# Kernel optimization log

Measured on AMD Instinct MI355X. Metric: run time of the kernel, lower is better.

Reference implementation:

```python
import jax, jax.numpy as jnp
import numpy as np

N = 50000
E = 1600000
IN = 128
HID = 128
OUT = 64
NL = 200000
NEG_SLOPE = 0.2


def _glorot(key, shape):
    fan_in, fan_out = shape[0], shape[-1]
    s = jnp.sqrt(6.0 / (fan_in + fan_out))
    return jax.random.uniform(key, shape, jnp.float32, -s, s)


def setup_inputs() -> dict:
    key = jax.random.key(0)
    ks = jax.random.split(key, 16)
    x = jax.random.normal(ks[0], (N, IN), jnp.float32)
    edge_index = jax.random.randint(ks[1], (2, E), 0, N, dtype=jnp.int32)
    edge_label_index = jax.random.randint(ks[2], (2, NL), 0, N, dtype=jnp.int32)
    return {
        "x": x,
        "edge_index": edge_index,
        "edge_label_index": edge_label_index,
        "W1": _glorot(ks[3], (IN, HID)),  "a1s": _glorot(ks[4], (HID,)),  "a1d": _glorot(ks[5], (HID,)),  "b1": jnp.zeros((HID,), jnp.float32),
        "W2": _glorot(ks[6], (HID, HID)), "a2s": _glorot(ks[7], (HID,)),  "a2d": _glorot(ks[8], (HID,)),  "b2": jnp.zeros((HID,), jnp.float32),
        "W3": _glorot(ks[9], (HID, HID)), "a3s": _glorot(ks[10], (HID,)), "a3d": _glorot(ks[11], (HID,)), "b3": jnp.zeros((HID,), jnp.float32),
        "W4": _glorot(ks[12], (HID, OUT)), "b4": jnp.zeros((OUT,), jnp.float32),
    }


def _add_self_loops(edge_index, n):
    loop = jnp.arange(n, dtype=edge_index.dtype)
    return jnp.concatenate([edge_index, jnp.stack([loop, loop])], axis=1)


def gat_conv(x, edge_index, W, a_s, a_d, b):
    """PyG GATConv, heads=1, add_self_loops=True: gather, LeakyReLU score,
    segment softmax over destination nodes, scatter-add aggregate."""
    n = x.shape[0]
    ei = _add_self_loops(edge_index, n)
    src, dst = ei[0], ei[1]
    h = x @ W                                    # [N, H]
    e = jax.nn.leaky_relu((h @ a_s)[src] + (h @ a_d)[dst], NEG_SLOPE)  # [E']
    m = jax.ops.segment_max(e, dst, num_segments=n)
    p = jnp.exp(e - m[dst])
    s = jax.ops.segment_sum(p, dst, num_segments=n)
    alpha = p / s[dst]                           # segment softmax
    out = jax.ops.segment_sum(h[src] * alpha[:, None], dst, num_segments=n)
    return out + b


def gcn_conv(x, edge_index, W, b):
    """PyG GCNConv: self-loops + symmetric degree normalization."""
    n = x.shape[0]
    ei = _add_self_loops(edge_index, n)
    src, dst = ei[0], ei[1]
    h = x @ W
    deg = jax.ops.segment_sum(jnp.ones(src.shape, h.dtype), dst, num_segments=n)
    dinv = jax.lax.rsqrt(deg)
    norm = dinv[src] * dinv[dst]                 # [E']
    out = jax.ops.segment_sum(h[src] * norm[:, None], dst, num_segments=n)
    return out + b


def reference(x, edge_index, edge_label_index,
              W1, a1s, a1d, b1, W2, a2s, a2d, b2,
              W3, a3s, a3d, b3, W4, b4):
    h = jax.nn.relu(gat_conv(x, edge_index, W1, a1s, a1d, b1))
    h = jax.nn.relu(gat_conv(h, edge_index, W2, a2s, a2d, b2))
    h = jax.nn.relu(gat_conv(h, edge_index, W3, a3s, a3d, b3))
    z = gcn_conv(h, edge_index, W4, b4)          # [N, OUT]
    # decode: dot product of endpoint embeddings -> link logits [NL]
    return (z[edge_label_index[0]] * z[edge_label_index[1]]).sum(axis=-1)
```

## Files before the change

kernel.cpp:

```cpp
#include <hip/hip_runtime.h>
#include <hip/hip_fp16.h>
#include <math.h>

#define NN   50000
#define NE   1600000
#define NLBL 200000
#define CAP  80
#define NEG  0.2f
#define NBK  196
#define CAPB 8800
#define CHK  4096
#define GBIN 391

typedef unsigned short u16;
typedef _Float16 half8 __attribute__((ext_vector_type(8)));
typedef float floatx4 __attribute__((ext_vector_type(4)));


__device__ void ph_bin(int blk, const int* __restrict__ ei,
                       int* __restrict__ gcnt, unsigned* __restrict__ bins) {
    __shared__ int cntL[NBK];
    __shared__ int offL[NBK];
    __shared__ int curL[NBK];
    __shared__ int curG[NBK];
    __shared__ unsigned stage[CHK];
    const int tid = threadIdx.x;
    const int e0 = blk * CHK + tid * 16;
    const bool act = (e0 + 15) < NE;

    unsigned pk[16];
    int bb[16];
    if (act) {
#pragma unroll
        for (int g = 0; g < 4; ++g) {
            int4 s4 = *(const int4*)&ei[e0 + g * 4];
            int4 d4 = *(const int4*)&ei[NE + e0 + g * 4];
            int sa[4] = {s4.x, s4.y, s4.z, s4.w};
            int da[4] = {d4.x, d4.y, d4.z, d4.w};
#pragma unroll
            for (int k = 0; k < 4; ++k) {
                int idx = g * 4 + k;
                bb[idx] = da[k] >> 8;
                pk[idx] = (unsigned)sa[k] | ((unsigned)(da[k] & 255) << 16)
                        | ((unsigned)bb[idx] << 24);
            }
        }
    }
    for (int i = tid; i < NBK; i += 256) cntL[i] = 0;
    __syncthreads();
    if (act) {
#pragma unroll
        for (int k = 0; k < 16; ++k) atomicAdd(&cntL[bb[k]], 1);
    }
    __syncthreads();
    if (tid < NBK) {
        int acc = 0;
        for (int i = 0; i < tid; ++i) acc += cntL[i];
        offL[tid] = acc;
        curL[tid] = acc;
    }
    __syncthreads();
    for (int i = tid; i < NBK; i += 256) curG[i] = atomicAdd(&gcnt[i], cntL[i]);
    __syncthreads();
    if (act) {
#pragma unroll
        for (int k = 0; k < 16; ++k) {
            int pos = atomicAdd(&curL[bb[k]], 1);
            stage[pos] = pk[k];
        }
    }
    __syncthreads();
    const int tot = offL[NBK - 1] + cntL[NBK - 1];
    for (int j = tid; j < tot; j += 256) {
        unsigned v = stage[j];
        int b = v >> 24;
        int lr = j - offL[b];
        bins[(size_t)b * CAPB + curG[b] + lr] = v & 0x00FFFFFFu;
    }
}

__global__ __launch_bounds__(256) void k_build(const unsigned* __restrict__ bins,
                                               const int* __restrict__ gcnt,
                                               int* __restrict__ cnt,
                                               u16* __restrict__ csr) {
    __shared__ u16 rows[256 * CAP];
    __shared__ int cur[256];
    const int b = blockIdx.x, tid = threadIdx.x;
    const int d0 = b << 8;
    const int nd = min(256, NN - d0);
    if (tid < nd) { cur[tid] = 1; rows[tid * CAP] = (u16)(d0 + tid); }
    __syncthreads();
    const int n = gcnt[b];
    for (int i = tid; i < n; i += 256) {
        unsigned v = bins[(size_t)b * CAPB + i];
        int s = v & 0xFFFF, dl = (v >> 16) & 0xFF;
        int pos = atomicAdd(&cur[dl], 1);
        if (pos < CAP) rows[dl * CAP + pos] = (u16)s;
    }
    __syncthreads();
    const unsigned* rw = (const unsigned*)rows;
    unsigned* cw = (unsigned*)(csr + (size_t)d0 * CAP);
    const int tot = nd * (CAP / 2);
    for (int i = tid; i < tot; i += 256) cw[i] = rw[i];
    if (tid < nd) cnt[d0 + tid] = cur[tid];
}


__global__ __launch_bounds__(256) void k_pre(const float* __restrict__ W1f,
                                             const float* __restrict__ W2f,
                                             const float* __restrict__ W3f,
                                             const float* __restrict__ W4f,
                                             half8* __restrict__ Wf1,
                                             half8* __restrict__ Wf2,
                                             half8* __restrict__ Wf3,
                                             half8* __restrict__ Wf4,
                                             int* __restrict__ gcnt) {
    if (blockIdx.x == 28) {
        int i = threadIdx.x;
        if (i < NBK) gcnt[i] = 0;
        return;
    }
    int e = blockIdx.x * 256 + threadIdx.x;
    const float* W;
    half8* Wf;
    int nout, le;
    if (e < 2048)      { W = W1f; Wf = Wf1; nout = 128; le = e; }
    else if (e < 4096) { W = W2f; Wf = Wf2; nout = 128; le = e - 2048; }
    else if (e < 6144) { W = W3f; Wf = Wf3; nout = 128; le = e - 4096; }
    else               { W = W4f; Wf = Wf4; nout = 64;  le = e - 6144; }
    int c = le >> 8, rem = le & 255, ks = rem >> 6, lane = rem & 63;
    int n = lane & 15, quad = lane >> 4;
    int col = c * 16 + n, k0 = ks * 32 + quad * 8;
    half8 v;
#pragma unroll
    for (int j = 0; j < 8; ++j) v[j] = (_Float16)W[(size_t)(k0 + j) * nout + col];
    Wf[le] = v;
}


template <int NOUT, bool ATTN, typename TA>
__device__ __forceinline__ void gemm_tile(int gt, int lane,
                                          const TA* __restrict__ A,
                                          const half8* __restrict__ Wf,
                                          __half* __restrict__ C,
                                          const float* __restrict__ a_s,
                                          const float* __restrict__ a_d,
                                          float* __restrict__ asv,
                                          float* __restrict__ adv) {
    constexpr int CT = NOUT / 16;
    constexpr int OSTR = (NOUT == 64) ? 64 : 128;
    const int n = lane & 15, quad = lane >> 4;
    if (gt * 16 >= NN) return;
    const int row = gt * 16 + n;

    half8 a[4];
#pragma unroll
    for (int ks = 0; ks < 4; ++ks) {
        int c128 = ks * 32 + quad * 8;
        if constexpr (sizeof(TA) == 2) {
            a[ks] = *(const half8*)((const _Float16*)A + (size_t)row * 128 + c128);
        } else {
            const float* Ap = (const float*)A + (size_t)row * 128 + c128;
            float4 f0 = *(const float4*)Ap;
            float4 f1 = *(const float4*)(Ap + 4);
            half8 v;
            v[0] = (_Float16)f0.x; v[1] = (_Float16)f0.y; v[2] = (_Float16)f0.z; v[3] = (_Float16)f0.w;
            v[4] = (_Float16)f1.x; v[5] = (_Float16)f1.y; v[6] = (_Float16)f1.z; v[7] = (_Float16)f1.w;
            a[ks] = v;
        }
    }

    floatx4 acc[CT];
#pragma unroll
    for (int c = 0; c < CT; ++c) acc[c] = (floatx4){0.f, 0.f, 0.f, 0.f};
#pragma unroll
    for (int c = 0; c < CT; ++c) {
#pragma unroll
        for (int ks = 0; ks < 4; ++ks) {
            half8 b = Wf[(c * 4 + ks) * 64 + lane];
            acc[c] = __builtin_amdgcn_mfma_f32_16x16x32_f16(b, a[ks], acc[c], 0, 0, 0);
        }
    }

#pragma unroll
    for (int c = 0; c < CT; ++c) {
        __half2 h0 = __floats2half2_rn(acc[c][0], acc[c][1]);
        __half2 h1 = __floats2half2_rn(acc[c][2], acc[c][3]);
        uint2 u;
        __builtin_memcpy(&u.x, &h0, 4);
        __builtin_memcpy(&u.y, &h1, 4);
        *(uint2*)&C[(size_t)row * OSTR + c * 16 + quad * 4] = u;
    }

    if (ATTN) {
        float ps = 0.f, pd = 0.f;
#pragma unroll
        for (int c = 0; c < CT; ++c) {
#pragma unroll
            for (int reg = 0; reg < 4; ++reg) {
                float w = acc[c][reg];
                ps = fmaf(w, a_s[c * 16 + quad * 4 + reg], ps);
                pd = fmaf(w, a_d[c * 16 + quad * 4 + reg], pd);
            }
        }
        ps += __shfl_xor(ps, 16); ps += __shfl_xor(ps, 32);
        pd += __shfl_xor(pd, 16); pd += __shfl_xor(pd, 32);
        if (quad == 0) { asv[row] = ps; adv[row] = pd; }
    }
}

__global__ __launch_bounds__(256) void k_bin_gemm1(const int* __restrict__ ei,
                                                   int* __restrict__ gcnt,
                                                   unsigned* __restrict__ bins,
                                                   const float* __restrict__ x,
                                                   const half8* __restrict__ Wf1,
                                                   __half* __restrict__ G,
                                                   const float* __restrict__ a_s,
                                                   const float* __restrict__ a_d,
                                                   float* __restrict__ asv,
                                                   float* __restrict__ adv) {
    if (blockIdx.x < GBIN) { ph_bin(blockIdx.x, ei, gcnt, bins); return; }
    int gt = (blockIdx.x - GBIN) * 4 + (threadIdx.x >> 6);
    gemm_tile<128, true, float>(gt, threadIdx.x & 63, x, Wf1, G, a_s, a_d, asv, adv);
}

template <int NOUT, bool ATTN>
__global__ __launch_bounds__(64) void k_gemm64(const __half* __restrict__ A,
                                               const half8* __restrict__ Wf,
                                               __half* __restrict__ C,
                                               const float* __restrict__ a_s,
                                               const float* __restrict__ a_d,
                                               float* __restrict__ asv,
                                               float* __restrict__ adv) {
    gemm_tile<NOUT, ATTN, __half>(blockIdx.x, threadIdx.x & 63, A, Wf, C,
                                  a_s, a_d, asv, adv);
}

__device__ __forceinline__ void fma_h8v(half8 h, float al, float* acc) {
#pragma unroll
    for (int k = 0; k < 8; ++k) acc[k] = fmaf(al, (float)h[k], acc[k]);
}


__global__ __launch_bounds__(256) void k_gat_agg(const __half* __restrict__ h,
                                                 const int* __restrict__ cnt,
                                                 const u16* __restrict__ csr,
                                                 const float* __restrict__ asv,
                                                 const float* __restrict__ adv,
                                                 const float* __restrict__ bias,
                                                 __half* __restrict__ out) {
    __shared__ float2 metaL[4][88];
    int lane = threadIdx.x & 63, wv = threadIdx.x >> 6;
    int d = blockIdx.x * 4 + wv;
    if (d >= NN) return;
    int deg = cnt[d]; if (deg > CAP) deg = CAP;
    const float advd = adv[d];
    const u16* rowp = csr + (size_t)d * CAP;

    int j0 = lane, j1 = lane + 64;
    int s0 = 0, s1 = 0;
    float e0 = -INFINITY, e1 = -INFINITY;
    if (j0 < deg) {
        s0 = rowp[j0];
        float t = asv[s0] + advd;
        e0 = (t >= 0.f) ? t : NEG * t;
    }
    if (j1 < deg) {
        s1 = rowp[j1];
        float t = asv[s1] + advd;
        e1 = (t >= 0.f) ? t : NEG * t;
    }
    float m = fmaxf(e0, e1);
#pragma unroll
    for (int off = 32; off; off >>= 1) m = fmaxf(m, __shfl_xor(m, off));
    float p0 = (j0 < deg) ? __expf(e0 - m) : 0.f;
    float p1 = (j1 < deg) ? __expf(e1 - m) : 0.f;
    float s = p0 + p1;
#pragma unroll
    for (int off = 32; off; off >>= 1) s += __shfl_xor(s, off);
    float inv = 1.f / s;
    metaL[wv][j0] = make_float2(p0 * inv, __int_as_float(s0));
    if (j1 < 88) metaL[wv][j1] = make_float2(p1 * inv, __int_as_float(s1));

    int slot = lane >> 4, r = lane & 15;
    const _Float16* hb = (const _Float16*)h + r * 8;
    float acc[8];
#pragma unroll
    for (int k = 0; k < 8; ++k) acc[k] = 0.f;
    int degp = (deg + 3) & ~3;
    int degM = deg & ~15;
    int base = 0;
    for (; base < degM; base += 16) {
        float al[4]; int sj[4];
#pragma unroll
        for (int u = 0; u < 4; ++u) {
            float2 ms = metaL[wv][base + u * 4 + slot];
            al[u] = ms.x; sj[u] = __float_as_int(ms.y);
        }
        half8 hv[4];
#pragma unroll
        for (int u = 0; u < 4; ++u) hv[u] = *(const half8*)(hb + (size_t)sj[u] * 128);
#pragma unroll
        for (int u = 0; u < 4; ++u) fma_h8v(hv[u], al[u], acc);
    }
    for (; base < degp; base += 4) {
        float2 ms = metaL[wv][base + slot];
        half8 hv = *(const half8*)(hb + (size_t)__float_as_int(ms.y) * 128);
        fma_h8v(hv, ms.x, acc);
    }
#pragma unroll
    for (int k = 0; k < 8; ++k) {
        acc[k] += __shfl_xor(acc[k], 16);
        acc[k] += __shfl_xor(acc[k], 32);
    }
    if (slot == 0) {
        __half2 ho[4];
#pragma unroll
        for (int k = 0; k < 4; ++k) {
            float oa = fmaxf(acc[2 * k]     + bias[r * 8 + 2 * k],     0.f);
            float ob = fmaxf(acc[2 * k + 1] + bias[r * 8 + 2 * k + 1], 0.f);
            ho[k] = __floats2half2_rn(oa, ob);
        }
        uint4 u;
        __builtin_memcpy(&u, &ho[0], 16);
        *(uint4*)&out[(size_t)d * 128 + r * 8] = u;
    }
}


__global__ __launch_bounds__(256) void k_gcn_agg(const __half* __restrict__ h,
                                                 const int* __restrict__ cnt,
                                                 const u16* __restrict__ csr,
                                                 const float* __restrict__ bias,
                                                 __half* __restrict__ z) {
    __shared__ float2 metaL[4][88];
    int lane = threadIdx.x & 63, wv = threadIdx.x >> 6;
    int d = blockIdx.x * 4 + wv;
    if (d >= NN) return;
    int degc = cnt[d];
    int deg = degc > CAP ? CAP : degc;
    float did = rsqrtf((float)degc);
    const u16* rowp = csr + (size_t)d * CAP;

    int j0 = lane, j1 = lane + 64;
    int s0 = 0, s1 = 0;
    float n0 = 0.f, n1 = 0.f;
    if (j0 < deg) { s0 = rowp[j0]; n0 = rsqrtf((float)cnt[s0]) * did; }
    if (j1 < deg) { s1 = rowp[j1]; n1 = rsqrtf((float)cnt[s1]) * did; }
    metaL[wv][j0] = make_float2(n0, __int_as_float(s0));
    if (j1 < 88) metaL[wv][j1] = make_float2(n1, __int_as_float(s1));

    int slot = lane >> 3, r = lane & 7;
    const _Float16* hb = (const _Float16*)h + r * 8;
    float acc[8];
#pragma unroll
    for (int k = 0; k < 8; ++k) acc[k] = 0.f;

    int degp = (deg + 7) & ~7;
    int degM = deg & ~15;
    int base = 0;
    for (; base < degM; base += 16) {
        float nm[2]; int sj[2];
#pragma unroll
        for (int u = 0; u < 2; ++u) {
            float2 ms = metaL[wv][base + u * 8 + slot];
            nm[u] = ms.x; sj[u] = __float_as_int(ms.y);
        }
        half8 hv[2];
#pragma unroll
        for (int u = 0; u < 2; ++u) hv[u] = *(const half8*)(hb + (size_t)sj[u] * 64);
#pragma unroll
        for (int u = 0; u < 2; ++u) fma_h8v(hv[u], nm[u], acc);
    }
    for (; base < degp; base += 8) {
        float2 ms = metaL[wv][base + slot];
        half8 hv = *(const half8*)(hb + (size_t)__float_as_int(ms.y) * 64);
        fma_h8v(hv, ms.x, acc);
    }
#pragma unroll
    for (int k = 0; k < 8; ++k) {
        acc[k] += __shfl_xor(acc[k], 8);
        acc[k] += __shfl_xor(acc[k], 16);
        acc[k] += __shfl_xor(acc[k], 32);
    }
    if (slot == 0) {
        __half2 ho[4];
#pragma unroll
        for (int k = 0; k < 4; ++k) {
            float oa = acc[2 * k]     + bias[r * 8 + 2 * k];
            float ob = acc[2 * k + 1] + bias[r * 8 + 2 * k + 1];
            ho[k] = __floats2half2_rn(oa, ob);
        }
        uint4 u;
        __builtin_memcpy(&u, &ho[0], 16);
        *(uint4*)&z[(size_t)d * 64 + r * 8] = u;
    }
}


__global__ __launch_bounds__(256) void k_decode(const __half* __restrict__ z,
                                                const int* __restrict__ eli,
                                                float* __restrict__ outp) {
    int lane = threadIdx.x & 63, wv = threadIdx.x >> 6;
    int g = lane >> 4, r = lane & 15;
    int idx = (blockIdx.x * 4 + wv) * 4 + g;
    if (idx >= NLBL) return;
    int a = eli[idx], b = eli[NLBL + idx];
    uint2 ua = *(const uint2*)&z[(size_t)a * 64 + r * 4];
    uint2 ub = *(const uint2*)&z[(size_t)b * 64 + r * 4];
    float2 a0 = __half22float2(*(__half2*)&ua.x);
    float2 a1 = __half22float2(*(__half2*)&ua.y);
    float2 b0 = __half22float2(*(__half2*)&ub.x);
    float2 b1 = __half22float2(*(__half2*)&ub.y);
    float v = a0.x * b0.x + a0.y * b0.y + a1.x * b1.x + a1.y * b1.y;
#pragma unroll
    for (int off = 8; off; off >>= 1) v += __shfl_xor(v, off);
    if (r == 0) outp[idx] = v;
}


extern "C" void kernel_launch(void* const* d_in, const int* in_sizes, int n_in,
                              void* d_out, int out_size, void* d_ws, size_t ws_size,
                              hipStream_t stream) {
    const float* x   = (const float*)d_in[0];
    const int*   ei  = (const int*)d_in[1];
    const int*   eli = (const int*)d_in[2];
    const float* W1 = (const float*)d_in[3];
    const float* a1s = (const float*)d_in[4];
    const float* a1d = (const float*)d_in[5];
    const float* b1 = (const float*)d_in[6];
    const float* W2 = (const float*)d_in[7];
    const float* a2s = (const float*)d_in[8];
    const float* a2d = (const float*)d_in[9];
    const float* b2 = (const float*)d_in[10];
    const float* W3 = (const float*)d_in[11];
    const float* a3s = (const float*)d_in[12];
    const float* a3d = (const float*)d_in[13];
    const float* b3 = (const float*)d_in[14];
    const float* W4 = (const float*)d_in[15];
    const float* b4 = (const float*)d_in[16];
    float* outp = (float*)d_out;

    char* p = (char*)d_ws;
    auto alloc = [&](size_t bytes) -> char* {
        char* r = p;
        p += (bytes + 255) & ~(size_t)255;
        return r;
    };
    int*    cnt  = (int*)alloc((size_t)NN * 4);
    u16*    csr  = (u16*)alloc((size_t)NN * CAP * 2);
    int*    gcnt = (int*)alloc((size_t)NBK * 4);
    float*  asv  = (float*)alloc((size_t)NN * 4);
    float*  advv = (float*)alloc((size_t)NN * 4);
    __half* G    = (__half*)alloc((size_t)NN * 128 * 2);
    __half* B1   = (__half*)alloc((size_t)NN * 128 * 2);
    __half* B2   = (__half*)alloc((size_t)NN * 128 * 2);
    __half* zf   = (__half*)alloc((size_t)NN * 64 * 2);
    half8*  Wf1  = (half8*)alloc(2048 * 16);
    half8*  Wf2  = (half8*)alloc(2048 * 16);
    half8*  Wf3  = (half8*)alloc(2048 * 16);
    half8*  Wf4  = (half8*)alloc(1024 * 16);
    unsigned* bins = (unsigned*)alloc((size_t)NBK * CAPB * 4);
    __half* H64  = B2;

    const int gG1   = GBIN + 782;
    const int gGemm = (NN + 15) / 16;
    const int gNode = (NN + 3) / 4;
    const int gDec  = (NLBL + 15) / 16;

    k_pre<<<29, 256, 0, stream>>>(W1, W2, W3, W4, Wf1, Wf2, Wf3, Wf4, gcnt);
    k_bin_gemm1<<<gG1, 256, 0, stream>>>(ei, gcnt, bins, x, Wf1, G, a1s, a1d, asv, advv);
    k_build<<<NBK, 256, 0, stream>>>(bins, gcnt, cnt, csr);

    k_gat_agg<<<gNode, 256, 0, stream>>>(G, cnt, csr, asv, advv, b1, B1);

    k_gemm64<128, true><<<gGemm, 64, 0, stream>>>(B1, Wf2, G, a2s, a2d, asv, advv);
    k_gat_agg<<<gNode, 256, 0, stream>>>(G, cnt, csr, asv, advv, b2, B2);

    k_gemm64<128, true><<<gGemm, 64, 0, stream>>>(B2, Wf3, G, a3s, a3d, asv, advv);
    k_gat_agg<<<gNode, 256, 0, stream>>>(G, cnt, csr, asv, advv, b3, B1);

    k_gemm64<64, false><<<gGemm, 64, 0, stream>>>(B1, Wf4, H64, nullptr, nullptr, nullptr, nullptr);
    k_gcn_agg<<<gNode, 256, 0, stream>>>(H64, cnt, csr, b4, zf);

    k_decode<<<gDec, 256, 0, stream>>>(zf, eli, outp);
}
```

Before: 375.1 us.

## Fuse GAT aggregation with the next layer's GEMM through a shared-memory tile

Each GAT aggregation block now handles 16 destination nodes (4 per wave), writes the ReLU'd fp16 rows into a shared-memory tile, then one wave runs the next layer's MFMA GEMM and attention projections on that tile. This removes three separate GEMM launches and the global round trip of the intermediate activations. In exchange, blocks are fewer and longer, with a sync and a single-wave GEMM tail that idles three waves. Score buffers are double-buffered so a layer can read its inputs while writing the next layer's.

```diff
diff --git a/kernel.cpp b/kernel.cpp
--- a/kernel.cpp
+++ b/kernel.cpp
@@ -138,9 +138,8 @@
 }
 
 
-template <int NOUT, bool ATTN, typename TA>
-__device__ __forceinline__ void gemm_tile(int gt, int lane,
-                                          const TA* __restrict__ A,
+template <int NOUT, bool ATTN>
+__device__ __forceinline__ void gemm_core(int rowbase, int lane, const half8* a,
                                           const half8* __restrict__ Wf,
                                           __half* __restrict__ C,
                                           const float* __restrict__ a_s,
@@ -150,25 +149,7 @@
     constexpr int CT = NOUT / 16;
     constexpr int OSTR = (NOUT == 64) ? 64 : 128;
     const int n = lane & 15, quad = lane >> 4;
-    if (gt * 16 >= NN) return;
-    const int row = gt * 16 + n;
-
-    half8 a[4];
-#pragma unroll
-    for (int ks = 0; ks < 4; ++ks) {
-        int c128 = ks * 32 + quad * 8;
-        if constexpr (sizeof(TA) == 2) {
-            a[ks] = *(const half8*)((const _Float16*)A + (size_t)row * 128 + c128);
-        } else {
-            const float* Ap = (const float*)A + (size_t)row * 128 + c128;
-            float4 f0 = *(const float4*)Ap;
-            float4 f1 = *(const float4*)(Ap + 4);
-            half8 v;
-            v[0] = (_Float16)f0.x; v[1] = (_Float16)f0.y; v[2] = (_Float16)f0.z; v[3] = (_Float16)f0.w;
-            v[4] = (_Float16)f1.x; v[5] = (_Float16)f1.y; v[6] = (_Float16)f1.z; v[7] = (_Float16)f1.w;
-            a[ks] = v;
-        }
-    }
+    const int row = rowbase + n;
 
     floatx4 acc[CT];
 #pragma unroll
@@ -221,19 +202,22 @@
                                                    float* __restrict__ adv) {
     if (blockIdx.x < GBIN) { ph_bin(blockIdx.x, ei, gcnt, bins); return; }
     int gt = (blockIdx.x - GBIN) * 4 + (threadIdx.x >> 6);
-    gemm_tile<128, true, float>(gt, threadIdx.x & 63, x, Wf1, G, a_s, a_d, asv, adv);
-}
-
-template <int NOUT, bool ATTN>
-__global__ __launch_bounds__(64) void k_gemm64(const __half* __restrict__ A,
-                                               const half8* __restrict__ Wf,
-                                               __half* __restrict__ C,
-                                               const float* __restrict__ a_s,
-                                               const float* __restrict__ a_d,
-                                               float* __restrict__ asv,
-                                               float* __restrict__ adv) {
-    gemm_tile<NOUT, ATTN, __half>(blockIdx.x, threadIdx.x & 63, A, Wf, C,
-                                  a_s, a_d, asv, adv);
+    if (gt * 16 >= NN) return;
+    int lane = threadIdx.x & 63;
+    int n = lane & 15, quad = lane >> 4;
+    int row = gt * 16 + n;
+    half8 a[4];
+#pragma unroll
+    for (int ks = 0; ks < 4; ++ks) {
+        const float* Ap = x + (size_t)row * 128 + ks * 32 + quad * 8;
+        float4 f0 = *(const float4*)Ap;
+        float4 f1 = *(const float4*)(Ap + 4);
+        half8 v;
+        v[0] = (_Float16)f0.x; v[1] = (_Float16)f0.y; v[2] = (_Float16)f0.z; v[3] = (_Float16)f0.w;
+        v[4] = (_Float16)f1.x; v[5] = (_Float16)f1.y; v[6] = (_Float16)f1.z; v[7] = (_Float16)f1.w;
+        a[ks] = v;
+    }
+    gemm_core<128, true>(gt * 16, lane, a, Wf1, G, a_s, a_d, asv, adv);
 }
 
 __device__ __forceinline__ void fma_h8v(half8 h, float al, float* acc) {
@@ -242,88 +226,107 @@
 }
 
 
-__global__ __launch_bounds__(256) void k_gat_agg(const __half* __restrict__ h,
-                                                 const int* __restrict__ cnt,
-                                                 const u16* __restrict__ csr,
-                                                 const float* __restrict__ asv,
-                                                 const float* __restrict__ adv,
-                                                 const float* __restrict__ bias,
-                                                 __half* __restrict__ out) {
+template <int NOUTN, bool ATTNN>
+__global__ __launch_bounds__(256) void k_agg_gemm(const __half* __restrict__ h,
+                                                  const int* __restrict__ cnt,
+                                                  const u16* __restrict__ csr,
+                                                  const float* __restrict__ asv_in,
+                                                  const float* __restrict__ adv_in,
+                                                  const float* __restrict__ bias,
+                                                  const half8* __restrict__ WfN,
+                                                  __half* __restrict__ Gout,
+                                                  const float* __restrict__ a_sN,
+                                                  const float* __restrict__ a_dN,
+                                                  float* __restrict__ asvN,
+                                                  float* __restrict__ advN) {
     __shared__ float2 metaL[4][88];
+    __shared__ __half tile[16][136];
     int lane = threadIdx.x & 63, wv = threadIdx.x >> 6;
-    int d = blockIdx.x * 4 + wv;
-    if (d >= NN) return;
-    int deg = cnt[d]; if (deg > CAP) deg = CAP;
-    const float advd = adv[d];
-    const u16* rowp = csr + (size_t)d * CAP;
-
-    int j0 = lane, j1 = lane + 64;
-    int s0 = 0, s1 = 0;
-    float e0 = -INFINITY, e1 = -INFINITY;
-    if (j0 < deg) {
-        s0 = rowp[j0];
-        float t = asv[s0] + advd;
-        e0 = (t >= 0.f) ? t : NEG * t;
-    }
-    if (j1 < deg) {
-        s1 = rowp[j1];
-        float t = asv[s1] + advd;
-        e1 = (t >= 0.f) ? t : NEG * t;
-    }
-    float m = fmaxf(e0, e1);
-#pragma unroll
-    for (int off = 32; off; off >>= 1) m = fmaxf(m, __shfl_xor(m, off));
-    float p0 = (j0 < deg) ? __expf(e0 - m) : 0.f;
-    float p1 = (j1 < deg) ? __expf(e1 - m) : 0.f;
-    float s = p0 + p1;
-#pragma unroll
-    for (int off = 32; off; off >>= 1) s += __shfl_xor(s, off);
-    float inv = 1.f / s;
-    metaL[wv][j0] = make_float2(p0 * inv, __int_as_float(s0));
-    if (j1 < 88) metaL[wv][j1] = make_float2(p1 * inv, __int_as_float(s1));
-
     int slot = lane >> 4, r = lane & 15;
     const _Float16* hb = (const _Float16*)h + r * 8;
-    float acc[8];
-#pragma unroll
-    for (int k = 0; k < 8; ++k) acc[k] = 0.f;
-    int degp = (deg + 3) & ~3;
-    int degM = deg & ~15;
-    int base = 0;
-    for (; base < degM; base += 16) {
-        float al[4]; int sj[4];
-#pragma unroll
-        for (int u = 0; u < 4; ++u) {
-            float2 ms = metaL[wv][base + u * 4 + slot];
-            al[u] = ms.x; sj[u] = __float_as_int(ms.y);
-        }
-        half8 hv[4];
-#pragma unroll
-        for (int u = 0; u < 4; ++u) hv[u] = *(const half8*)(hb + (size_t)sj[u] * 128);
-#pragma unroll
-        for (int u = 0; u < 4; ++u) fma_h8v(hv[u], al[u], acc);
-    }
-    for (; base < degp; base += 4) {
-        float2 ms = metaL[wv][base + slot];
-        half8 hv = *(const half8*)(hb + (size_t)__float_as_int(ms.y) * 128);
-        fma_h8v(hv, ms.x, acc);
-    }
-#pragma unroll
-    for (int k = 0; k < 8; ++k) {
-        acc[k] += __shfl_xor(acc[k], 16);
-        acc[k] += __shfl_xor(acc[k], 32);
-    }
-    if (slot == 0) {
-        __half2 ho[4];
-#pragma unroll
-        for (int k = 0; k < 4; ++k) {
-            float oa = fmaxf(acc[2 * k]     + bias[r * 8 + 2 * k],     0.f);
-            float ob = fmaxf(acc[2 * k + 1] + bias[r * 8 + 2 * k + 1], 0.f);
-            ho[k] = __floats2half2_rn(oa, ob);
-        }
-        uint4 u;
-        __builtin_memcpy(&u, &ho[0], 16);
-        *(uint4*)&out[(size_t)d * 128 + r * 8] = u;
+
+    for (int q = 0; q < 4; ++q) {
+        int d = blockIdx.x * 16 + wv * 4 + q;
+        int deg = cnt[d]; if (deg > CAP) deg = CAP;
+        const float advd = adv_in[d];
+        const u16* rowp = csr + (size_t)d * CAP;
+
+        int j0 = lane, j1 = lane + 64;
+        int s0 = 0, s1 = 0;
+        float e0 = -INFINITY, e1 = -INFINITY;
+        if (j0 < deg) {
+            s0 = rowp[j0];
+            float t = asv_in[s0] + advd;
+            e0 = (t >= 0.f) ? t : NEG * t;
+        }
+        if (j1 < deg) {
+            s1 = rowp[j1];
+            float t = asv_in[s1] + advd;
+            e1 = (t >= 0.f) ? t : NEG * t;
+        }
+        float m = fmaxf(e0, e1);
+#pragma unroll
+        for (int off = 32; off; off >>= 1) m = fmaxf(m, __shfl_xor(m, off));
+        float p0 = (j0 < deg) ? __expf(e0 - m) : 0.f;
+        float p1 = (j1 < deg) ? __expf(e1 - m) : 0.f;
+        float s = p0 + p1;
+#pragma unroll
+        for (int off = 32; off; off >>= 1) s += __shfl_xor(s, off);
+        float inv = 1.f / s;
+        metaL[wv][j0] = make_float2(p0 * inv, __int_as_float(s0));
+        if (j1 < 88) metaL[wv][j1] = make_float2(p1 * inv, __int_as_float(s1));
+
+        float acc[8];
+#pragma unroll
+        for (int k = 0; k < 8; ++k) acc[k] = 0.f;
+        int degp = (deg + 3) & ~3;
+        int degM = deg & ~15;
+        int base = 0;
+        for (; base < degM; base += 16) {
+            float al[4]; int sj[4];
+#pragma unroll
+            for (int u = 0; u < 4; ++u) {
+                float2 ms = metaL[wv][base + u * 4 + slot];
+                al[u] = ms.x; sj[u] = __float_as_int(ms.y);
+            }
+            half8 hv[4];
+#pragma unroll
+            for (int u = 0; u < 4; ++u) hv[u] = *(const half8*)(hb + (size_t)sj[u] * 128);
+#pragma unroll
+            for (int u = 0; u < 4; ++u) fma_h8v(hv[u], al[u], acc);
+        }
+        for (; base < degp; base += 4) {
+            float2 ms = metaL[wv][base + slot];
+            half8 hv = *(const half8*)(hb + (size_t)__float_as_int(ms.y) * 128);
+            fma_h8v(hv, ms.x, acc);
+        }
+#pragma unroll
+        for (int k = 0; k < 8; ++k) {
+            acc[k] += __shfl_xor(acc[k], 16);
+            acc[k] += __shfl_xor(acc[k], 32);
+        }
+        if (slot == 0) {
+            __half2 ho[4];
+#pragma unroll
+            for (int k = 0; k < 4; ++k) {
+                float oa = fmaxf(acc[2 * k]     + bias[r * 8 + 2 * k],     0.f);
+                float ob = fmaxf(acc[2 * k + 1] + bias[r * 8 + 2 * k + 1], 0.f);
+                ho[k] = __floats2half2_rn(oa, ob);
+            }
+            uint4 u;
+            __builtin_memcpy(&u, &ho[0], 16);
+            *(uint4*)&tile[wv * 4 + q][r * 8] = u;
+        }
+    }
+    __syncthreads();
+    if (wv == 0) {
+        int n = lane & 15, quad = lane >> 4;
+        half8 a[4];
+#pragma unroll
+        for (int ks = 0; ks < 4; ++ks)
+            a[ks] = *(const half8*)&tile[n][ks * 32 + quad * 8];
+        gemm_core<NOUTN, ATTNN>(blockIdx.x * 16, lane, a, WfN, Gout,
+                                a_sN, a_dN, asvN, advN);
     }
 }
 
@@ -450,37 +453,36 @@
     int*    cnt  = (int*)alloc((size_t)NN * 4);
     u16*    csr  = (u16*)alloc((size_t)NN * CAP * 2);
     int*    gcnt = (int*)alloc((size_t)NBK * 4);
-    float*  asv  = (float*)alloc((size_t)NN * 4);
-    float*  advv = (float*)alloc((size_t)NN * 4);
-    __half* G    = (__half*)alloc((size_t)NN * 128 * 2);
-    __half* B1   = (__half*)alloc((size_t)NN * 128 * 2);
-    __half* B2   = (__half*)alloc((size_t)NN * 128 * 2);
+    float*  asv1 = (float*)alloc((size_t)NN * 4);
+    float*  adv1 = (float*)alloc((size_t)NN * 4);
+    float*  asv2 = (float*)alloc((size_t)NN * 4);
+    float*  adv2 = (float*)alloc((size_t)NN * 4);
+    __half* Ga   = (__half*)alloc((size_t)NN * 128 * 2);
+    __half* Gb   = (__half*)alloc((size_t)NN * 128 * 2);
     __half* zf   = (__half*)alloc((size_t)NN * 64 * 2);
     half8*  Wf1  = (half8*)alloc(2048 * 16);
     half8*  Wf2  = (half8*)alloc(2048 * 16);
     half8*  Wf3  = (half8*)alloc(2048 * 16);
     half8*  Wf4  = (half8*)alloc(1024 * 16);
     unsigned* bins = (unsigned*)alloc((size_t)NBK * CAPB * 4);
-    __half* H64  = B2;
+    __half* H64  = Gb;
 
     const int gG1   = GBIN + 782;
-    const int gGemm = (NN + 15) / 16;
+    const int gAgg  = NN / 16;
     const int gNode = (NN + 3) / 4;
     const int gDec  = (NLBL + 15) / 16;
 
     k_pre<<<29, 256, 0, stream>>>(W1, W2, W3, W4, Wf1, Wf2, Wf3, Wf4, gcnt);
-    k_bin_gemm1<<<gG1, 256, 0, stream>>>(ei, gcnt, bins, x, Wf1, G, a1s, a1d, asv, advv);
+    k_bin_gemm1<<<gG1, 256, 0, stream>>>(ei, gcnt, bins, x, Wf1, Ga, a1s, a1d, asv1, adv1);
     k_build<<<NBK, 256, 0, stream>>>(bins, gcnt, cnt, csr);
 
-    k_gat_agg<<<gNode, 256, 0, stream>>>(G, cnt, csr, asv, advv, b1, B1);
-
-    k_gemm64<128, true><<<gGemm, 64, 0, stream>>>(B1, Wf2, G, a2s, a2d, asv, advv);
-    k_gat_agg<<<gNode, 256, 0, stream>>>(G, cnt, csr, asv, advv, b2, B2);
-
-    k_gemm64<128, true><<<gGemm, 64, 0, stream>>>(B2, Wf3, G, a3s, a3d, asv, advv);
-    k_gat_agg<<<gNode, 256, 0, stream>>>(G, cnt, csr, asv, advv, b3, B1);
-
-    k_gemm64<64, false><<<gGemm, 64, 0, stream>>>(B1, Wf4, H64, nullptr, nullptr, nullptr, nullptr);
+    k_agg_gemm<128, true><<<gAgg, 256, 0, stream>>>(Ga, cnt, csr, asv1, adv1, b1,
+                                                    Wf2, Gb, a2s, a2d, asv2, adv2);
+    k_agg_gemm<128, true><<<gAgg, 256, 0, stream>>>(Gb, cnt, csr, asv2, adv2, b2,
+                                                    Wf3, Ga, a3s, a3d, asv1, adv1);
+    k_agg_gemm<64, false><<<gAgg, 256, 0, stream>>>(Ga, cnt, csr, asv1, adv1, b3,
+                                                    Wf4, H64, nullptr, nullptr, nullptr, nullptr);
+
     k_gcn_agg<<<gNode, 256, 0, stream>>>(H64, cnt, csr, b4, zf);
 
     k_decode<<<gDec, 256, 0, stream>>>(zf, eli, outp);
```

Measured after the change: 385.7 us. +2.8%, slower.
